# Kernel tuning notes

Measured on AMD Instinct MI355X. Metric: run time of the kernel, lower is better.

## Reference

```python
import jax, jax.numpy as jnp
import numpy as np

N = 50000; IN_DIM = 128; HID = 128; T = 4; R = 3; E = 500000

def setup_inputs() -> dict:
    key = jax.random.key(0)
    ks = jax.random.split(key, 20)
    def nrm(k, shape, s):
        return jax.random.normal(k, shape, jnp.float32) * s
    s_in = 1.0 / float(np.sqrt(IN_DIM)); s_h = 1.0 / float(np.sqrt(HID))
    return {
        'feat_seq': nrm(ks[0], (T, N, IN_DIM), 1.0),
        'src': jax.random.randint(ks[1], (T, R, E), 0, N, jnp.int32),
        'dst': jax.random.randint(ks[2], (T, R, E), 0, N, jnp.int32),
        'ew': jax.random.uniform(ks[3], (T, R, E), jnp.float32),
        'W_in': nrm(ks[4], (IN_DIM, HID), s_in), 'b_in': jnp.zeros((HID,), jnp.float32),
        'W1': nrm(ks[5], (R, HID, HID), s_h), 'b1': jnp.zeros((R, HID), jnp.float32),
        'W2': nrm(ks[6], (R, HID, HID), s_h), 'b2': jnp.zeros((R, HID), jnp.float32),
        'q1': nrm(ks[7], (HID,), 1.0), 'q2': nrm(ks[8], (HID,), 1.0),
        'ln1_g': jnp.ones((HID,), jnp.float32), 'ln1_b': jnp.zeros((HID,), jnp.float32),
        'ln2_g': jnp.ones((HID,), jnp.float32), 'ln2_b': jnp.zeros((HID,), jnp.float32),
        'gWih': nrm(ks[9], (HID, 3 * HID), s_h), 'gbih': jnp.zeros((3 * HID,), jnp.float32),
        'gWhh': nrm(ks[10], (HID, 3 * HID), s_h), 'gbhh': jnp.zeros((3 * HID,), jnp.float32),
        'temp_q': nrm(ks[11], (HID,), 1.0),
        'tW1': nrm(ks[12], (IN_DIM, HID), s_in), 'tb1': jnp.zeros((HID,), jnp.float32),
        'tW2': nrm(ks[13], (HID, HID), s_h), 'tb2': jnp.zeros((HID,), jnp.float32),
        'cW1': nrm(ks[14], (3 * HID, HID), 1.0 / float(np.sqrt(3 * HID))), 'cb1': jnp.zeros((HID,), jnp.float32),
        'cW2': nrm(ks[15], (HID, 1), s_h), 'cb2': jnp.zeros((1,), jnp.float32),
    }

def _ln(x, g, b):
    m = x.mean(-1, keepdims=True)
    v = ((x - m) ** 2).mean(-1, keepdims=True)
    return (x - m) * jax.lax.rsqrt(v + 1e-5) * g + b

def _rel_attn(stack, q):
    # stack: [R,N,H]; tanh-softmax attention over relations
    score = jnp.einsum('rnh,h->rn', jnp.tanh(stack), q)
    alpha = jax.nn.softmax(score, axis=0)
    return jnp.einsum('rn,rnh->nh', alpha, stack)

def _conv(x, s, d, w, Wr, br):
    # DGL GraphConv norm='right' with edge_weight: mean-by-in-degree weighted SpMM
    msg = w[:, None] * x[s]                                   # [E,H]
    agg = jax.ops.segment_sum(msg, d, num_segments=N)
    deg = jax.ops.segment_sum(jnp.ones_like(w), d, num_segments=N)
    return (agg / jnp.maximum(deg, 1.0)[:, None]) @ Wr + br

def reference(feat_seq, src, dst, ew, W_in, b_in, W1, b1, W2, b2, q1, q2, ln1_g, ln1_b, ln2_g, ln2_b, gWih, gbih, gWhh, gbhh, temp_q, tW1, tb1, tW2, tb2, cW1, cb1, cW2, cb2):
    conv_all = jax.vmap(_conv, in_axes=(None, 0, 0, 0, 0, 0))
    def spatial(x, s, d, w):
        h0 = jax.nn.relu(x @ W_in + b_in)
        h1 = _ln(h0 + jax.nn.relu(_rel_attn(conv_all(h0, s, d, w, W1, b1), q1)), ln1_g, ln1_b)
        h2 = _ln(h1 + jax.nn.relu(_rel_attn(conv_all(h1, s, d, w, W2, b2), q2)), ln2_g, ln2_b)
        return h2
    hs = jnp.stack([spatial(feat_seq[t], src[t], dst[t], ew[t]) for t in range(T)], axis=0)  # [T,N,H]
    def gru_step(h, x):
        gi = x @ gWih + gbih
        gh = h @ gWhh + gbhh
        ir, iz, inn = jnp.split(gi, 3, axis=-1)
        hr, hz, hn = jnp.split(gh, 3, axis=-1)
        r = jax.nn.sigmoid(ir + hr)
        zg = jax.nn.sigmoid(iz + hz)
        n = jnp.tanh(inn + r * hn)
        hnew = (1.0 - zg) * n + zg * h
        return hnew, hnew
    _, outs = jax.lax.scan(gru_step, jnp.zeros((N, HID), feat_seq.dtype), hs)  # [T,N,H]
    out = jnp.transpose(outs, (1, 0, 2))                       # [N,T,H]
    last = out[:, -1, :]
    t_score = jnp.einsum('nth,h->nt', jnp.tanh(out), temp_q)
    t_alpha = jax.nn.softmax(t_score, axis=1)
    attn = jnp.einsum('nt,nth->nh', t_alpha, out)
    tab = jax.nn.relu(jax.nn.relu(feat_seq[-1] @ tW1 + tb1) @ tW2 + tb2)
    z = jnp.concatenate([last, attn, tab], axis=-1)
    return (jax.nn.relu(z @ cW1 + cb1) @ cW2 + cb2)[:, 0]       # [N]
```

## Files before the change

kernel.cpp:

```cpp
#include <hip/hip_runtime.h>
#include <hip/hip_bf16.h>
#include <math.h>

#define NN 50000
#define TT 4
#define RR 3
#define EE 500000
#define RANGE 6400
#define NRANGE 8

typedef __attribute__((ext_vector_type(8))) short bf16x8;
typedef __attribute__((ext_vector_type(4))) float f32x4;

__device__ inline unsigned short f2b(float f)
{
    union { __hip_bfloat16 h; unsigned short u; } cv;
    cv.h = __float2bfloat16(f);
    return cv.u;
}
__device__ inline float b2f(unsigned short u)
{
    union { unsigned int u; float f; } cv;
    cv.u = ((unsigned int)u) << 16;
    return cv.f;
}
__device__ inline bf16x8 pack8(float4 a, float4 b)
{
    bf16x8 r;
    r[0] = (short)f2b(a.x); r[1] = (short)f2b(a.y); r[2] = (short)f2b(a.z); r[3] = (short)f2b(a.w);
    r[4] = (short)f2b(b.x); r[5] = (short)f2b(b.y); r[6] = (short)f2b(b.z); r[7] = (short)f2b(b.w);
    return r;
}


__global__ __launch_bounds__(256)
void diag_kernel(float* __restrict__ out, float v)
{
    int i = blockIdx.x * 256 + threadIdx.x;
    if (i < NN) out[i] = v;
}


__global__ __launch_bounds__(256)
void wswz_kernel(const float* __restrict__ W, unsigned short* __restrict__ dst, int C, int S)
{
    int idx = blockIdx.x * 256 + threadIdx.x;
    int per = 128 * C;
    if (idx >= S * per) return;
    int s = idx / per, rem = idx - s * per;
    int j = rem & 7;
    int lane = (rem >> 3) & 63;
    int blk = rem >> 9;
    int ncg = C >> 4;
    int kc = blk / ncg, cg = blk - kc * ncg;
    int k = kc * 32 + (lane >> 4) * 8 + j;
    int c = cg * 16 + (lane & 15);
    dst[idx] = f2b(W[(size_t)s * 128 * C + (size_t)k * C + c]);
}


__global__ __launch_bounds__(1024)
void count_hist(const int* __restrict__ dst, int* __restrict__ cnt)
{
    __shared__ int hist[RANGE];
    const int g = blockIdx.y;
    const int r0 = blockIdx.x * RANGE;
    for (int i = threadIdx.x; i < RANGE; i += 1024) hist[i] = 0;
    __syncthreads();
    const int4* d4 = (const int4*)(dst + (size_t)g * EE);
    for (int i = threadIdx.x; i < EE / 4; i += 1024) {
        int4 v = d4[i];
        int a0 = v.x - r0; if ((unsigned)a0 < (unsigned)RANGE) atomicAdd(&hist[a0], 1);
        int a1 = v.y - r0; if ((unsigned)a1 < (unsigned)RANGE) atomicAdd(&hist[a1], 1);
        int a2 = v.z - r0; if ((unsigned)a2 < (unsigned)RANGE) atomicAdd(&hist[a2], 1);
        int a3 = v.w - r0; if ((unsigned)a3 < (unsigned)RANGE) atomicAdd(&hist[a3], 1);
    }
    __syncthreads();
    int* c = cnt + (size_t)g * NN;
    for (int i = threadIdx.x; i < RANGE; i += 1024) {
        int n = r0 + i;
        if (n < NN) c[n] = hist[i];
    }
}

__global__ __launch_bounds__(1024)
void scan_kernel(int* __restrict__ cnt, int* __restrict__ rows)
{
    int g = blockIdx.x;
    int tid = threadIdx.x;
    const int CH = (NN + 1023) / 1024;
    int s0 = tid * CH;
    int s1 = s0 + CH; if (s1 > NN) s1 = NN;
    int* c = cnt + (size_t)g * NN;
    int* ro = rows + (size_t)g * (NN + 1);
    int sum = 0;
    for (int i = s0; i < s1; ++i) sum += c[i];
    __shared__ int sd[1024];
    sd[tid] = sum;
    __syncthreads();
    for (int off = 1; off < 1024; off <<= 1) {
        int v = 0;
        if (tid >= off) v = sd[tid - off];
        __syncthreads();
        sd[tid] += v;
        __syncthreads();
    }
    int total = sd[1023];
    int prefix = (tid == 0) ? 0 : sd[tid - 1];
    for (int i = s0; i < s1; ++i) {
        int cv = c[i];
        ro[i] = prefix;
        c[i] = prefix;
        prefix += cv;
    }
    if (tid == 0) ro[NN] = total;
}


__global__ __launch_bounds__(256)
void fill_kernel(const int* __restrict__ src, const int* __restrict__ dst,
                 const float* __restrict__ ew, int* __restrict__ cur,
                 int2* __restrict__ srcw)
{
    int g = blockIdx.y;
    int e = blockIdx.x * 256 + threadIdx.x;
    if (e >= EE) return;
    size_t idx = (size_t)g * EE + e;
    int d = dst[idx];
    int pos = atomicAdd(&cur[(size_t)g * NN + d], 1);
    int2 p;
    p.x = src[idx];
    p.y = __float_as_int(ew[idx]);
    srcw[(size_t)g * EE + pos] = p;
}


__global__ __launch_bounds__(256)
void agg16_kernel(const unsigned short* __restrict__ x16,
                  const int2* __restrict__ srcw,
                  const int* __restrict__ rows,
                  unsigned short* __restrict__ agg16)
{
    int wid = (blockIdx.x * 256 + threadIdx.x) >> 6;
    int lane = threadIdx.x & 63;
    if (wid >= RR * NN) return;
    int r = wid / NN;
    int n = wid - r * NN;
    const int* rs = rows + (size_t)r * (NN + 1);
    int e0 = rs[n], e1 = rs[n + 1];
    const int2* sw = srcw + (size_t)r * EE;
    const int co = lane * 2;
    float ax = 0.f, ay = 0.f;
    for (int e = e0; e < e1; e += 16) {
        int2 p[16];
        unsigned int v[16];
#pragma unroll
        for (int i = 0; i < 16; ++i) {
            int idx = (e + i < e1) ? e + i : e1 - 1;
            p[i] = sw[idx];
        }
#pragma unroll
        for (int i = 0; i < 16; ++i)
            v[i] = *(const unsigned int*)(x16 + (size_t)p[i].x * 128 + co);
#pragma unroll
        for (int i = 0; i < 16; ++i) {
            float w = (e + i < e1) ? __int_as_float(p[i].y) : 0.f;
            ax += w * b2f((unsigned short)(v[i] & 0xffffu));
            ay += w * b2f((unsigned short)(v[i] >> 16));
        }
    }
    float inv = 1.0f / fmaxf((float)(e1 - e0), 1.0f);
    unsigned int o = (unsigned int)f2b(ax * inv) | ((unsigned int)f2b(ay * inv) << 16);
    *(unsigned int*)(agg16 + ((size_t)r * NN + n) * 128 + co) = o;
}


__global__ __launch_bounds__(256)
void mmb(const void* in, int in_bf16, long in_zs, int ldin,
         const unsigned short* __restrict__ Ws, long w_zs,
         const float* __restrict__ bias, long b_zs,
         float* out, long out_zs, int ldout,
         unsigned short* out16, long out16_zs,
         int rows, int act)
{
    const int tid = threadIdx.x;
    const int wv = tid >> 6, l = tid & 63;
    const int z = blockIdx.z;
    const int r0 = blockIdx.x * 64 + wv * 16;
    const int lk = (l >> 4) * 8;
    int rowA = r0 + (l & 15);
    int rowc = rowA < rows ? rowA : rows - 1;

    bf16x8 a[4];
    if (in_bf16) {
        const unsigned short* inb = (const unsigned short*)in + (size_t)z * in_zs
                                    + (size_t)rowc * ldin + lk;
#pragma unroll
        for (int kc = 0; kc < 4; ++kc) {
            uint4 u = *(const uint4*)(inb + kc * 32);
            a[kc] = *(bf16x8*)&u;
        }
    } else {
        const float* inf = (const float*)in + (size_t)z * in_zs
                           + (size_t)rowc * ldin + lk;
#pragma unroll
        for (int kc = 0; kc < 4; ++kc) {
            float4 u0 = *(const float4*)(inf + kc * 32);
            float4 u1 = *(const float4*)(inf + kc * 32 + 4);
            a[kc] = pack8(u0, u1);
        }
    }

    const unsigned short* Wz = Ws + (size_t)z * w_zs;
    const float* bz = bias + (size_t)z * b_zs;
    float* oz = out ? out + (size_t)z * out_zs : (float*)0;
    unsigned short* o16z = out16 ? out16 + (size_t)z * out16_zs : (unsigned short*)0;
    const int colbase = l & 15;
    const int rbase = r0 + (l >> 4) * 4;

#pragma unroll
    for (int cg = 0; cg < 8; ++cg) {
        f32x4 acc = {0.f, 0.f, 0.f, 0.f};
#pragma unroll
        for (int kc = 0; kc < 4; ++kc) {
            uint4 bu = *(const uint4*)(Wz + ((size_t)(kc * 8 + cg) * 64 + l) * 8);
            acc = __builtin_amdgcn_mfma_f32_16x16x32_bf16(a[kc], *(bf16x8*)&bu, acc, 0, 0, 0);
        }
        int col = cg * 16 + colbase;
        float bvv = bz[col];
#pragma unroll
        for (int j = 0; j < 4; ++j) {
            int gr = rbase + j;
            if (gr >= rows) continue;
            float v = acc[j] + bvv;
            if (act) v = fmaxf(v, 0.f);
            if (oz) oz[(size_t)gr * ldout + col] = v;
            if (o16z) o16z[(size_t)gr * 128 + col] = f2b(v);
        }
    }
}


__global__ __launch_bounds__(256)
void grub4(float* HS,
           const unsigned short* __restrict__ Wis, const float* __restrict__ bi,
           const unsigned short* __restrict__ Whs, const float* __restrict__ bh)
{
    __shared__ __align__(16) unsigned short hbuf[4][16 * 136];
    const int tid = threadIdx.x;
    const int wv = tid >> 6, l = tid & 63;
    const int r0 = blockIdx.x * 64 + wv * 16;
    const int lo = l & 15, hi = l >> 4;
    const int lk = hi * 8;
    const int rowc = (r0 + lo) < NN ? (r0 + lo) : NN - 1;
    const int rbase = r0 + hi * 4;
    unsigned short* hb = hbuf[wv];

    for (int i = l; i < 16 * 136; i += 64) hb[i] = 0;

    float hold[8][4];
#pragma unroll
    for (int cg = 0; cg < 8; ++cg)
#pragma unroll
        for (int j = 0; j < 4; ++j) hold[cg][j] = 0.f;

#pragma unroll 1
    for (int t = 0; t < TT; ++t) {
        float* xt = HS + (size_t)t * NN * 128;
        bf16x8 ax[4], hx[4];
        const float* bx = xt + (size_t)rowc * 128 + lk;
#pragma unroll
        for (int kc = 0; kc < 4; ++kc) {
            ax[kc] = pack8(*(const float4*)(bx + kc * 32), *(const float4*)(bx + kc * 32 + 4));
            uint4 hu = *(const uint4*)(hb + lo * 136 + kc * 32 + lk);
            hx[kc] = *(bf16x8*)&hu;
        }

#pragma unroll 1
        for (int cg = 0; cg < 8; ++cg) {
            f32x4 air = {0.f,0.f,0.f,0.f}, ahr = {0.f,0.f,0.f,0.f};
            f32x4 aiz = {0.f,0.f,0.f,0.f}, ahz = {0.f,0.f,0.f,0.f};
            f32x4 ain = {0.f,0.f,0.f,0.f}, ahn = {0.f,0.f,0.f,0.f};
#pragma unroll
            for (int kc = 0; kc < 4; ++kc) {
                uint4 br = *(const uint4*)(Wis + ((size_t)(kc * 24 + 0 + cg) * 64 + l) * 8);
                uint4 hr = *(const uint4*)(Whs + ((size_t)(kc * 24 + 0 + cg) * 64 + l) * 8);
                uint4 bz = *(const uint4*)(Wis + ((size_t)(kc * 24 + 8 + cg) * 64 + l) * 8);
                uint4 hz = *(const uint4*)(Whs + ((size_t)(kc * 24 + 8 + cg) * 64 + l) * 8);
                uint4 bn = *(const uint4*)(Wis + ((size_t)(kc * 24 + 16 + cg) * 64 + l) * 8);
                uint4 hn = *(const uint4*)(Whs + ((size_t)(kc * 24 + 16 + cg) * 64 + l) * 8);
                air = __builtin_amdgcn_mfma_f32_16x16x32_bf16(ax[kc], *(bf16x8*)&br, air, 0, 0, 0);
                ahr = __builtin_amdgcn_mfma_f32_16x16x32_bf16(hx[kc], *(bf16x8*)&hr, ahr, 0, 0, 0);
                aiz = __builtin_amdgcn_mfma_f32_16x16x32_bf16(ax[kc], *(bf16x8*)&bz, aiz, 0, 0, 0);
                ahz = __builtin_amdgcn_mfma_f32_16x16x32_bf16(hx[kc], *(bf16x8*)&hz, ahz, 0, 0, 0);
                ain = __builtin_amdgcn_mfma_f32_16x16x32_bf16(ax[kc], *(bf16x8*)&bn, ain, 0, 0, 0);
                ahn = __builtin_amdgcn_mfma_f32_16x16x32_bf16(hx[kc], *(bf16x8*)&hn, ahn, 0, 0, 0);
            }
            int col = cg * 16 + lo;
            float bir = bi[col],       bhr = bh[col];
            float biz = bi[128 + col], bhz = bh[128 + col];
            float bin = bi[256 + col], bhn = bh[256 + col];
#pragma unroll
            for (int j = 0; j < 4; ++j) {
                float r_ = 1.f / (1.f + __expf(-(air[j] + bir + ahr[j] + bhr)));
                float z_ = 1.f / (1.f + __expf(-(aiz[j] + biz + ahz[j] + bhz)));
                float n_ = tanhf(ain[j] + bin + r_ * (ahn[j] + bhn));
                float o = (1.f - z_) * n_ + z_ * hold[cg][j];
                hold[cg][j] = o;
                int gr = rbase + j;
                if (gr < NN) xt[(size_t)gr * 128 + col] = o;
                hb[(hi * 4 + j) * 136 + col] = f2b(o);
            }
        }
    }
}


__global__ __launch_bounds__(256)
void cls_mfma(const float* __restrict__ in,
              const unsigned short* __restrict__ Ws,
              const float* __restrict__ b1_,
              const float* __restrict__ w2,
              const float* __restrict__ b2_,
              float* __restrict__ outv, int rows)
{
    const int tid = threadIdx.x;
    const int wv = tid >> 6, l = tid & 63;
    const int r0 = blockIdx.x * 64 + wv * 16;
    const int lk = (l >> 4) * 8;
    int rowA = r0 + (l & 15);
    int rowc = rowA < rows ? rowA : rows - 1;

    bf16x8 a[12];
    {
        const float* inf = in + (size_t)rowc * 384 + lk;
#pragma unroll
        for (int kc = 0; kc < 12; ++kc) {
            float4 u0 = *(const float4*)(inf + kc * 32);
            float4 u1 = *(const float4*)(inf + kc * 32 + 4);
            a[kc] = pack8(u0, u1);
        }
    }
    const int colbase = l & 15;
    const int rbase = r0 + (l >> 4) * 4;
    float part[4] = {0.f, 0.f, 0.f, 0.f};

#pragma unroll
    for (int cg = 0; cg < 8; ++cg) {
        f32x4 acc = {0.f, 0.f, 0.f, 0.f};
#pragma unroll
        for (int kc = 0; kc < 12; ++kc) {
            uint4 bu = *(const uint4*)(Ws + ((size_t)(kc * 8 + cg) * 64 + l) * 8);
            acc = __builtin_amdgcn_mfma_f32_16x16x32_bf16(a[kc], *(bf16x8*)&bu, acc, 0, 0, 0);
        }
        int col = cg * 16 + colbase;
        float b1v = b1_[col];
        float w2v = w2[col];
#pragma unroll
        for (int j = 0; j < 4; ++j)
            part[j] += fmaxf(acc[j] + b1v, 0.f) * w2v;
    }
    const float cb2v = b2_[0];
#pragma unroll
    for (int j = 0; j < 4; ++j) {
#pragma unroll
        for (int m = 1; m < 16; m <<= 1) part[j] += __shfl_xor(part[j], m);
        int gr = rbase + j;
        if ((l & 15) == 0 && gr < rows) outv[gr] = part[j] + cb2v;
    }
}


__device__ inline float wred(float v)
{
#pragma unroll
    for (int m = 32; m; m >>= 1) v += __shfl_xor(v, m);
    return v;
}

__global__ __launch_bounds__(256)
void attnln_kernel(const unsigned short* __restrict__ agg16,
                   const unsigned short* hin16,
                   const float* __restrict__ q,
                   const float* __restrict__ g,
                   const float* __restrict__ b,
                   float* hout,
                   unsigned short* hout16)
{
    int wid = (blockIdx.x * 256 + threadIdx.x) >> 6;
    int lane = threadIdx.x & 63;
    if (wid >= NN) return;
    int n = wid;
    float2 qv = *(const float2*)(q + lane * 2);
    float sx[3], sy[3], sc[3];
#pragma unroll
    for (int r = 0; r < 3; ++r) {
        unsigned int v = *(const unsigned int*)(agg16 + ((size_t)r * NN + n) * 128 + lane * 2);
        sx[r] = b2f((unsigned short)(v & 0xffffu));
        sy[r] = b2f((unsigned short)(v >> 16));
        sc[r] = wred(tanhf(sx[r]) * qv.x + tanhf(sy[r]) * qv.y);
    }
    float mx = fmaxf(sc[0], fmaxf(sc[1], sc[2]));
    float e0 = __expf(sc[0] - mx), e1 = __expf(sc[1] - mx), e2 = __expf(sc[2] - mx);
    float isum = 1.f / (e0 + e1 + e2);
    float axv = (e0 * sx[0] + e1 * sx[1] + e2 * sx[2]) * isum;
    float ayv = (e0 * sy[0] + e1 * sy[1] + e2 * sy[2]) * isum;
    unsigned int hv = *(const unsigned int*)(hin16 + (size_t)n * 128 + lane * 2);
    float ux = b2f((unsigned short)(hv & 0xffffu)) + fmaxf(axv, 0.f);
    float uy = b2f((unsigned short)(hv >> 16)) + fmaxf(ayv, 0.f);
    float mean = wred(ux + uy) * (1.f / 128.f);
    float dx = ux - mean, dy = uy - mean;
    float var = wred(dx * dx + dy * dy) * (1.f / 128.f);
    float rstd = rsqrtf(var + 1e-5f);
    float2 gv = *(const float2*)(g + lane * 2);
    float2 bv = *(const float2*)(b + lane * 2);
    float ox = dx * rstd * gv.x + bv.x;
    float oy = dy * rstd * gv.y + bv.y;
    if (hout) {
        float2 o; o.x = ox; o.y = oy;
        *(float2*)(hout + (size_t)n * 128 + lane * 2) = o;
    }
    if (hout16) {
        unsigned int p = (unsigned int)f2b(ox) | ((unsigned int)f2b(oy) << 16);
        *(unsigned int*)(hout16 + (size_t)n * 128 + lane * 2) = p;
    }
}


__global__ __launch_bounds__(256)
void temporal_kernel(const float* __restrict__ outs,
                     const float* __restrict__ tq,
                     float* __restrict__ zbuf)
{
    int wid = (blockIdx.x * 256 + threadIdx.x) >> 6;
    int lane = threadIdx.x & 63;
    if (wid >= NN) return;
    int n = wid;
    float2 qv = *(const float2*)(tq + lane * 2);
    float2 o[4];
    float sc[4];
#pragma unroll
    for (int t = 0; t < 4; ++t) {
        o[t] = *(const float2*)(outs + ((size_t)t * NN + n) * 128 + lane * 2);
        sc[t] = wred(tanhf(o[t].x) * qv.x + tanhf(o[t].y) * qv.y);
    }
    float mx = fmaxf(fmaxf(sc[0], sc[1]), fmaxf(sc[2], sc[3]));
    float e[4];
    float sum = 0.f;
#pragma unroll
    for (int t = 0; t < 4; ++t) { e[t] = __expf(sc[t] - mx); sum += e[t]; }
    float isum = 1.f / sum;
    float axv = 0.f, ayv = 0.f;
#pragma unroll
    for (int t = 0; t < 4; ++t) { axv += e[t] * o[t].x; ayv += e[t] * o[t].y; }
    axv *= isum; ayv *= isum;
    float* zr = zbuf + (size_t)n * 384;
    *(float2*)(zr + lane * 2) = o[3];
    float2 at; at.x = axv; at.y = ayv;
    *(float2*)(zr + 128 + lane * 2) = at;
}


extern "C" void kernel_launch(void* const* d_in, const int* in_sizes, int n_in,
                              void* d_out, int out_size, void* d_ws, size_t ws_size,
                              hipStream_t stream)
{
    const float* feat = (const float*)d_in[0];
    const int* srcp   = (const int*)d_in[1];
    const int* dstp   = (const int*)d_in[2];
    const float* ewp  = (const float*)d_in[3];
    const float* W_in = (const float*)d_in[4];
    const float* b_in = (const float*)d_in[5];
    const float* W1   = (const float*)d_in[6];
    const float* b1   = (const float*)d_in[7];
    const float* W2   = (const float*)d_in[8];
    const float* b2   = (const float*)d_in[9];
    const float* q1   = (const float*)d_in[10];
    const float* q2   = (const float*)d_in[11];
    const float* ln1g = (const float*)d_in[12];
    const float* ln1b = (const float*)d_in[13];
    const float* ln2g = (const float*)d_in[14];
    const float* ln2b = (const float*)d_in[15];
    const float* gWih = (const float*)d_in[16];
    const float* gbih = (const float*)d_in[17];
    const float* gWhh = (const float*)d_in[18];
    const float* gbhh = (const float*)d_in[19];
    const float* tq   = (const float*)d_in[20];
    const float* tW1  = (const float*)d_in[21];
    const float* tb1  = (const float*)d_in[22];
    const float* tW2  = (const float*)d_in[23];
    const float* tb2  = (const float*)d_in[24];
    const float* cW1  = (const float*)d_in[25];
    const float* cb1  = (const float*)d_in[26];
    const float* cW2  = (const float*)d_in[27];
    const float* cb2  = (const float*)d_in[28];
    float* outv = (float*)d_out;
    (void)in_sizes; (void)n_in; (void)out_size;

    const size_t o_HS    = 0;
    const size_t o_POOL  = 102400000;
    const size_t o_AGG16 = o_POOL;
    const size_t o_H16   = o_POOL + 38400000;
    const size_t o_SRCW  = o_POOL + 51200000;
    const size_t o_ROWS  = o_POOL + 99200000;
    const size_t o_CURS  = o_POOL + 101600128;
    const size_t o_ZB    = o_POOL;
    const size_t o_TAB   = o_POOL + 76800000;
    const size_t o_WSZ   = o_POOL + 104000128;
    const size_t NEED    = o_WSZ + 589824;

    if (ws_size < NEED) {
        diag_kernel<<<dim3((NN + 255) / 256), dim3(256), 0, stream>>>(outv, (float)(ws_size >> 20));
        return;
    }

    char* wsb = (char*)d_ws;
    float* HS             = (float*)(wsb + o_HS);
    unsigned short* AGG16 = (unsigned short*)(wsb + o_AGG16);
    unsigned short* H16   = (unsigned short*)(wsb + o_H16);
    int2*  SRCW           = (int2*)(wsb + o_SRCW);
    int*   ROWS           = (int*)(wsb + o_ROWS);
    int*   CURS           = (int*)(wsb + o_CURS);
    float* ZB             = (float*)(wsb + o_ZB);
    unsigned short* TAB16 = (unsigned short*)(wsb + o_TAB);
    unsigned short* WSZ   = (unsigned short*)(wsb + o_WSZ);

    unsigned short* Wins  = WSZ;
    unsigned short* W1s   = WSZ + 16384;
    unsigned short* W2s   = WSZ + 65536;
    unsigned short* gWihs = WSZ + 114688;
    unsigned short* gWhhs = WSZ + 163840;
    unsigned short* tW1s  = WSZ + 212992;
    unsigned short* tW2s  = WSZ + 229376;
    unsigned short* cW1s  = WSZ + 245760;

    const dim3 blk(256);
    const int G64 = (NN + 63) / 64;

    wswz_kernel<<<dim3((1 * 16384 + 255) / 256), blk, 0, stream>>>(W_in, Wins, 128, 1);
    wswz_kernel<<<dim3((3 * 16384 + 255) / 256), blk, 0, stream>>>(W1,   W1s,  128, 3);
    wswz_kernel<<<dim3((3 * 16384 + 255) / 256), blk, 0, stream>>>(W2,   W2s,  128, 3);
    wswz_kernel<<<dim3((1 * 49152 + 255) / 256), blk, 0, stream>>>(gWih, gWihs, 384, 1);
    wswz_kernel<<<dim3((1 * 49152 + 255) / 256), blk, 0, stream>>>(gWhh, gWhhs, 384, 1);
    wswz_kernel<<<dim3((1 * 16384 + 255) / 256), blk, 0, stream>>>(tW1,  tW1s, 128, 1);
    wswz_kernel<<<dim3((1 * 16384 + 255) / 256), blk, 0, stream>>>(tW2,  tW2s, 128, 1);
    wswz_kernel<<<dim3((3 * 16384 + 255) / 256), blk, 0, stream>>>(cW1,  cW1s, 128, 3);

    count_hist<<<dim3(NRANGE, TT * RR), dim3(1024), 0, stream>>>(dstp, CURS);
    scan_kernel<<<dim3(TT * RR), dim3(1024), 0, stream>>>(CURS, ROWS);
    fill_kernel<<<dim3((EE + 255) / 256, TT * RR), blk, 0, stream>>>(srcp, dstp, ewp, CURS, SRCW);

    for (int t = 0; t < TT; ++t) {
        mmb<<<dim3(G64, 1, 1), blk, 0, stream>>>(
            (const void*)(feat + (size_t)t * NN * 128), 0, 0, 128,
            Wins, 0, b_in, 0, (float*)0, 0, 0, H16, 0, NN, 1);

        for (int layer = 0; layer < 2; ++layer) {
            const unsigned short* Wls = layer ? W2s : W1s;
            const float* bl = layer ? b2 : b1;
            const float* ql = layer ? q2 : q1;
            const float* lg = layer ? ln2g : ln1g;
            const float* lb = layer ? ln2b : ln1b;
            float* hout = layer ? (HS + (size_t)t * NN * 128) : (float*)0;
            unsigned short* hout16 = layer ? (unsigned short*)0 : H16;

            agg16_kernel<<<dim3((RR * NN) / 4), blk, 0, stream>>>(
                H16, SRCW + (size_t)t * RR * EE, ROWS + (size_t)t * RR * (NN + 1), AGG16);
            mmb<<<dim3(G64, 1, RR), blk, 0, stream>>>(
                (const void*)AGG16, 1, (long)NN * 128, 128,
                Wls, 16384, bl, 128, (float*)0, 0, 0, AGG16, (long)NN * 128, NN, 0);
            attnln_kernel<<<dim3(NN / 4), blk, 0, stream>>>(
                AGG16, H16, ql, lg, lb, hout, hout16);
        }
    }

    grub4<<<dim3(G64), blk, 0, stream>>>(HS, gWihs, gbih, gWhhs, gbhh);

    temporal_kernel<<<dim3(NN / 4), blk, 0, stream>>>(HS, tq, ZB);

    mmb<<<dim3(G64, 1, 1), blk, 0, stream>>>(
        (const void*)(feat + (size_t)3 * NN * 128), 0, 0, 128,
        tW1s, 0, tb1, 0, (float*)0, 0, 0, TAB16, 0, NN, 1);
    mmb<<<dim3(G64, 1, 1), blk, 0, stream>>>(
        (const void*)TAB16, 1, 0, 128,
        tW2s, 0, tb2, 0, ZB + 256, 0, 384, (unsigned short*)0, 0, NN, 1);

    cls_mfma<<<dim3(G64), blk, 0, stream>>>(ZB, cW1s, cb1, cW2, cb2, outv, NN);
}
```

Baseline: 1.993 ms.

## Fuse per-relation GEMM with relation attention and LayerNorm into one kernel

```diff
diff --git a/kernel.cpp b/kernel.cpp
--- a/kernel.cpp
+++ b/kernel.cpp
@@ -242,6 +242,116 @@
 
 
 __global__ __launch_bounds__(256)
+void convln2(const unsigned short* __restrict__ agg16,
+             const unsigned short* hin16,
+             const unsigned short* __restrict__ Ws,
+             const float* __restrict__ bias,
+             const float* __restrict__ q,
+             const float* __restrict__ lg,
+             const float* __restrict__ lb,
+             float* hout,
+             unsigned short* hout16)
+{
+    __shared__ __align__(16) unsigned short st[4][3][16 * 132];
+    const int tid = threadIdx.x;
+    const int wv = tid >> 6, l = tid & 63;
+    const int r0 = blockIdx.x * 64 + wv * 16;
+    const int lo = l & 15, hi = l >> 4;
+    const int lk = hi * 8;
+    const int rowc = (r0 + lo) < NN ? (r0 + lo) : NN - 1;
+    const int rbase = r0 + hi * 4;
+
+    float sc[3][4];
+
+#pragma unroll 1
+    for (int r = 0; r < 3; ++r) {
+        bf16x8 a[4];
+        const unsigned short* inb = agg16 + ((size_t)r * NN + rowc) * 128 + lk;
+#pragma unroll
+        for (int kc = 0; kc < 4; ++kc) {
+            uint4 u = *(const uint4*)(inb + kc * 32);
+            a[kc] = *(bf16x8*)&u;
+        }
+        const unsigned short* Wz = Ws + (size_t)r * 16384;
+        unsigned short* sr = &st[wv][r][0];
+        float scj[4] = {0.f, 0.f, 0.f, 0.f};
+#pragma unroll 1
+        for (int cg = 0; cg < 8; ++cg) {
+            f32x4 acc = {0.f, 0.f, 0.f, 0.f};
+#pragma unroll
+            for (int kc = 0; kc < 4; ++kc) {
+                uint4 bu = *(const uint4*)(Wz + ((size_t)(kc * 8 + cg) * 64 + l) * 8);
+                acc = __builtin_amdgcn_mfma_f32_16x16x32_bf16(a[kc], *(bf16x8*)&bu, acc, 0, 0, 0);
+            }
+            int col = cg * 16 + lo;
+            float bv = bias[r * 128 + col];
+            float qv = q[col];
+#pragma unroll
+            for (int j = 0; j < 4; ++j) {
+                float v = acc[j] + bv;
+                scj[j] += tanhf(v) * qv;
+                sr[(hi * 4 + j) * 132 + col] = f2b(v);
+            }
+        }
+#pragma unroll
+        for (int j = 0; j < 4; ++j) {
+            float p = scj[j];
+#pragma unroll
+            for (int m = 1; m < 16; m <<= 1) p += __shfl_xor(p, m);
+            sc[r][j] = p;
+        }
+    }
+
+#pragma unroll 1
+    for (int j = 0; j < 4; ++j) {
+        int gr = rbase + j;
+        int grc = gr < NN ? gr : NN - 1;
+        float mx = fmaxf(sc[0][j], fmaxf(sc[1][j], sc[2][j]));
+        float e0 = __expf(sc[0][j] - mx), e1 = __expf(sc[1][j] - mx), e2 = __expf(sc[2][j] - mx);
+        float isum = 1.f / (e0 + e1 + e2);
+        float a0 = e0 * isum, a1 = e1 * isum, a2 = e2 * isum;
+        const int roff = (hi * 4 + j) * 132;
+
+        float u[8];
+        float msum = 0.f;
+#pragma unroll
+        for (int cg = 0; cg < 8; ++cg) {
+            int col = cg * 16 + lo;
+            float v0 = b2f(st[wv][0][roff + col]);
+            float v1 = b2f(st[wv][1][roff + col]);
+            float v2 = b2f(st[wv][2][roff + col]);
+            float av = a0 * v0 + a1 * v1 + a2 * v2;
+            float hv = b2f(hin16[(size_t)grc * 128 + col]);
+            u[cg] = hv + fmaxf(av, 0.f);
+            msum += u[cg];
+        }
+#pragma unroll
+        for (int m = 1; m < 16; m <<= 1) msum += __shfl_xor(msum, m);
+        float mean = msum * (1.f / 128.f);
+        float vsum = 0.f;
+#pragma unroll
+        for (int cg = 0; cg < 8; ++cg) {
+            float d = u[cg] - mean;
+            vsum += d * d;
+        }
+#pragma unroll
+        for (int m = 1; m < 16; m <<= 1) vsum += __shfl_xor(vsum, m);
+        float rstd = rsqrtf(vsum * (1.f / 128.f) + 1e-5f);
+
+        if (gr < NN) {
+#pragma unroll
+            for (int cg = 0; cg < 8; ++cg) {
+                int col = cg * 16 + lo;
+                float o = (u[cg] - mean) * rstd * lg[col] + lb[col];
+                if (hout)   hout[(size_t)gr * 128 + col] = o;
+                if (hout16) hout16[(size_t)gr * 128 + col] = f2b(o);
+            }
+        }
+    }
+}
+
+
+__global__ __launch_bounds__(256)
 void grub4(float* HS,
            const unsigned short* __restrict__ Wis, const float* __restrict__ bi,
            const unsigned short* __restrict__ Whs, const float* __restrict__ bh)
@@ -377,55 +487,6 @@
     for (int m = 32; m; m >>= 1) v += __shfl_xor(v, m);
     return v;
 }
-
-__global__ __launch_bounds__(256)
-void attnln_kernel(const unsigned short* __restrict__ agg16,
-                   const unsigned short* hin16,
-                   const float* __restrict__ q,
-                   const float* __restrict__ g,
-                   const float* __restrict__ b,
-                   float* hout,
-                   unsigned short* hout16)
-{
-    int wid = (blockIdx.x * 256 + threadIdx.x) >> 6;
-    int lane = threadIdx.x & 63;
-    if (wid >= NN) return;
-    int n = wid;
-    float2 qv = *(const float2*)(q + lane * 2);
-    float sx[3], sy[3], sc[3];
-#pragma unroll
-    for (int r = 0; r < 3; ++r) {
-        unsigned int v = *(const unsigned int*)(agg16 + ((size_t)r * NN + n) * 128 + lane * 2);
-        sx[r] = b2f((unsigned short)(v & 0xffffu));
-        sy[r] = b2f((unsigned short)(v >> 16));
-        sc[r] = wred(tanhf(sx[r]) * qv.x + tanhf(sy[r]) * qv.y);
-    }
-    float mx = fmaxf(sc[0], fmaxf(sc[1], sc[2]));
-    float e0 = __expf(sc[0] - mx), e1 = __expf(sc[1] - mx), e2 = __expf(sc[2] - mx);
-    float isum = 1.f / (e0 + e1 + e2);
-    float axv = (e0 * sx[0] + e1 * sx[1] + e2 * sx[2]) * isum;
-    float ayv = (e0 * sy[0] + e1 * sy[1] + e2 * sy[2]) * isum;
-    unsigned int hv = *(const unsigned int*)(hin16 + (size_t)n * 128 + lane * 2);
-    float ux = b2f((unsigned short)(hv & 0xffffu)) + fmaxf(axv, 0.f);
-    float uy = b2f((unsigned short)(hv >> 16)) + fmaxf(ayv, 0.f);
-    float mean = wred(ux + uy) * (1.f / 128.f);
-    float dx = ux - mean, dy = uy - mean;
-    float var = wred(dx * dx + dy * dy) * (1.f / 128.f);
-    float rstd = rsqrtf(var + 1e-5f);
-    float2 gv = *(const float2*)(g + lane * 2);
-    float2 bv = *(const float2*)(b + lane * 2);
-    float ox = dx * rstd * gv.x + bv.x;
-    float oy = dy * rstd * gv.y + bv.y;
-    if (hout) {
-        float2 o; o.x = ox; o.y = oy;
-        *(float2*)(hout + (size_t)n * 128 + lane * 2) = o;
-    }
-    if (hout16) {
-        unsigned int p = (unsigned int)f2b(ox) | ((unsigned int)f2b(oy) << 16);
-        *(unsigned int*)(hout16 + (size_t)n * 128 + lane * 2) = p;
-    }
-}
-
 
 __global__ __launch_bounds__(256)
 void temporal_kernel(const float* __restrict__ outs,
@@ -566,11 +627,8 @@
 
             agg16_kernel<<<dim3((RR * NN) / 4), blk, 0, stream>>>(
                 H16, SRCW + (size_t)t * RR * EE, ROWS + (size_t)t * RR * (NN + 1), AGG16);
-            mmb<<<dim3(G64, 1, RR), blk, 0, stream>>>(
-                (const void*)AGG16, 1, (long)NN * 128, 128,
-                Wls, 16384, bl, 128, (float*)0, 0, 0, AGG16, (long)NN * 128, NN, 0);
-            attnln_kernel<<<dim3(NN / 4), blk, 0, stream>>>(
-                AGG16, H16, ql, lg, lb, hout, hout16);
+            convln2<<<dim3(G64), blk, 0, stream>>>(
+                AGG16, H16, Wls, bl, ql, lg, lb, hout, hout16);
         }
     }
 
```

Measured after the change: 2.201 ms. 1.1x slower.
